# Kernel tuning notes

Hardware: AMD Instinct MI355X
Metric: run time of the kernel (lower is better)

The kernel has to match this reference:

```python
import jax, jax.numpy as jnp
import numpy as np

B, I, L, D, E, H, HR, A = 4096, 512, 128, 512, 8, 512, 256, 32


def setup_inputs() -> dict:
    key = jax.random.key(0)
    ks = jax.random.split(key, 12)
    s = 0.05
    n = lambda k, shape: (jax.random.normal(k, shape, jnp.float32) * s)
    return {
        "x": jax.random.normal(ks[0], (B, I), jnp.float32),
        "lang_embs": jax.random.normal(ks[1], (B, L), jnp.float32),
        "h_router": jnp.zeros((B, HR), jnp.float32),
        "h_experts": jnp.zeros((E, B, H), jnp.float32),
        # input projection Linear(I+L -> D)
        "W_in": n(ks[2], (D, I + L)), "b_in": jnp.zeros((D,), jnp.float32),
        # router GRU cell (PyTorch layout: rows ordered [r, z, n])
        "Wih_r": n(ks[3], (3 * HR, D)), "Whh_r": n(ks[4], (3 * HR, HR)),
        "bih_r": jnp.zeros((3 * HR,), jnp.float32), "bhh_r": jnp.zeros((3 * HR,), jnp.float32),
        # router fc Linear(HR -> E)
        "W_fc": n(ks[5], (E, HR)), "b_fc": jnp.zeros((E,), jnp.float32),
        # stacked expert GRU cells
        "Wih_e": n(ks[6], (E, 3 * H, D)), "Whh_e": n(ks[7], (E, 3 * H, H)),
        "bih_e": jnp.zeros((E, 3 * H), jnp.float32), "bhh_e": jnp.zeros((E, 3 * H), jnp.float32),
        # stacked expert projections Linear(H -> D)
        "W_proj": n(ks[8], (E, D, H)), "b_proj": jnp.zeros((E, D), jnp.float32),
        # head Linear(D -> A)
        "W_head": n(ks[9], (A, D)), "b_head": jnp.zeros((A,), jnp.float32),
    }


def _gru_cell(gx, gh, h):
    """Single GRU step given precomputed input/hidden gate pre-activations.
    gx, gh: (..., 3H) ordered [r, z, n]; h: (..., H)."""
    Hh = h.shape[-1]
    r = jax.nn.sigmoid(gx[..., :Hh] + gh[..., :Hh])
    z = jax.nn.sigmoid(gx[..., Hh:2 * Hh] + gh[..., Hh:2 * Hh])
    nct = jnp.tanh(gx[..., 2 * Hh:] + r * gh[..., 2 * Hh:])
    return (1.0 - z) * nct + z * h


def reference(x, lang_embs, h_router, h_experts,
              W_in, b_in, Wih_r, Whh_r, bih_r, bhh_r, W_fc, b_fc,
              Wih_e, Whh_e, bih_e, bhh_e, W_proj, b_proj, W_head, b_head):
    # input projection: (B, I+L) -> (B, D)
    xp = jnp.concatenate([x, lang_embs], axis=1) @ W_in.T + b_in

    # router GRU step + softmax weights
    gx_r = xp @ Wih_r.T + bih_r                      # (B, 3HR)
    gh_r = h_router @ Whh_r.T + bhh_r                # (B, 3HR)
    h_router_new = _gru_cell(gx_r, gh_r, h_router)   # (B, HR)
    weights = jax.nn.softmax(h_router_new @ W_fc.T + b_fc, axis=-1)  # (B, E)

    # all expert GRU steps fused into batched einsums over the expert dim
    gx_e = jnp.einsum('bd,egd->ebg', xp, Wih_e) + bih_e[:, None, :]        # (E, B, 3H)
    gh_e = jnp.einsum('ebh,egh->ebg', h_experts, Whh_e) + bhh_e[:, None, :]
    h_experts_new = _gru_cell(gx_e, gh_e, h_experts)                        # (E, B, H)

    # per-expert projection back to intermediate dim, then router-weighted sum
    expert_out = jnp.einsum('ebh,edh->ebd', h_experts_new, W_proj) + b_proj[:, None, :]
    combined = jnp.einsum('ebd,be->bd', expert_out, weights)               # (B, D)

    logits = combined @ W_head.T + b_head                                  # (B, A)
    return (logits, h_router_new, h_experts_new)
```

## Files before the change

### kernel.cpp

```cpp
#include <hip/hip_runtime.h>
#include <cstddef>
#include <cstdint>

#define B_  4096
#define I_  512
#define L_  128
#define D_  512
#define E_  8
#define H_  512
#define HR_ 256
#define A_  32

typedef __attribute__((ext_vector_type(8))) __bf16 bf16x8;
typedef __attribute__((ext_vector_type(4))) __bf16 bf16x4;
typedef __attribute__((ext_vector_type(4))) float floatx4;

__device__ __forceinline__ float sigmoidf_(float x) { return 1.0f / (1.0f + __expf(-x)); }

__device__ __forceinline__ void load_lds16(const void* g, void* l) {
    __builtin_amdgcn_global_load_lds((__attribute__((address_space(1))) void*)g,
                                     (__attribute__((address_space(3))) void*)l, 16, 0, 0);
}

struct HiLo { __bf16 h, l; };
__device__ __forceinline__ HiLo hi_lo(float v) {
    HiLo r;
    r.h = (__bf16)v;
    r.l = (__bf16)(v - (float)r.h);
    return r;
}
__device__ __forceinline__ void split4(float4 v, bf16x4& hi, bf16x4& lo) {
    HiLo a = hi_lo(v.x), b = hi_lo(v.y), c = hi_lo(v.z), d = hi_lo(v.w);
    hi = (bf16x4){a.h, b.h, c.h, d.h};
    lo = (bf16x4){a.l, b.l, c.l, d.l};
}

__device__ __forceinline__ int stage_seg(int lane) {
    return (lane & 3) ^ ((lane >> 3) & 3);
}
__device__ __forceinline__ int frag_off(int lane) {
    const int r = lane & 15, q = lane >> 4;
    return (r * 4 + (q ^ ((r >> 1) & 3))) * 8;
}

__global__ __launch_bounds__(256) void f2b_k(const float* __restrict__ src,
                                             __bf16* __restrict__ dst, int n4) {
    int i = blockIdx.x * 256 + threadIdx.x;
    if (i < n4) {
        float4 v = ((const float4*)src)[i];
        bf16x4 o = { (__bf16)v.x, (__bf16)v.y, (__bf16)v.z, (__bf16)v.w };
        *(bf16x4*)(dst + (size_t)i * 4) = o;
    }
}

__global__ __launch_bounds__(256) void wcat2_k(const float* __restrict__ W,
                                               __bf16* __restrict__ out,
                                               int K4, int n4tot) {
    int i4 = blockIdx.x * 256 + threadIdx.x;
    if (i4 >= n4tot) return;
    int row = i4 / K4;
    int c4  = i4 - row * K4;
    const int K = K4 * 4;
    float4 v = ((const float4*)W)[i4];
    bf16x4 hi, lo;
    split4(v, hi, lo);
    __bf16* dst = out + (size_t)row * 2 * K + c4 * 4;
    *(bf16x4*)(dst)     = hi;
    *(bf16x4*)(dst + K) = lo;
}

__global__ __launch_bounds__(256) void concat_cat_k(const float* __restrict__ x,
                                                    const float* __restrict__ lang,
                                                    __bf16* __restrict__ out) {
    int idx = blockIdx.x * 256 + threadIdx.x;
    int b = idx / 160;
    int c = idx - b * 160;
    float4 v;
    if (c < 128) v = ((const float4*)x)[(size_t)b * 128 + c];
    else         v = ((const float4*)lang)[(size_t)b * 32 + (c - 128)];
    bf16x4 hi, lo;
    split4(v, hi, lo);
    __bf16* dst = out + (size_t)b * 1920 + c * 4;
    *(bf16x4*)(dst)        = hi;
    *(bf16x4*)(dst + 640)  = hi;
    *(bf16x4*)(dst + 1280) = lo;
}

__global__ __launch_bounds__(256) void split2cat_k(const float* __restrict__ src,
                                                   __bf16* __restrict__ out) {
    int i4 = blockIdx.x * 256 + threadIdx.x;
    int b = i4 >> 7;
    int c4 = i4 & 127;
    float4 v = ((const float4*)src)[i4];
    bf16x4 hi, lo;
    split4(v, hi, lo);
    __bf16* dst = out + (size_t)b * 1536 + c4 * 4;
    *(bf16x4*)(dst)         = hi;
    *(bf16x4*)(dst + 512)   = hi;
    *(bf16x4*)(dst + 1024)  = lo;
}

__global__ __launch_bounds__(256) void f2bhe_k(const float* __restrict__ he,
                                               __bf16* __restrict__ dst, int r0) {
    int i4 = blockIdx.x * 256 + threadIdx.x;
    int e   = i4 >> 18;
    int rem = i4 & 262143;
    int row = rem >> 7;
    int c4  = rem & 127;
    float4 v = ((const float4*)he)[(size_t)e * (B_ * 128) + (size_t)(r0 + row) * 128 + c4];
    bf16x4 o = { (__bf16)v.x, (__bf16)v.y, (__bf16)v.z, (__bf16)v.w };
    *(bf16x4*)(dst + (size_t)i4 * 4) = o;
}

template<int MODE, bool XORD>
__global__ __launch_bounds__(256) void mgemm(
    const __bf16* __restrict__ A, long long aBatch,
    const __bf16* __restrict__ Bw, long long bBatch, int bRS, int kWrap,
    const float* __restrict__ bias, long long biasBatch,
    float* __restrict__ Cv, long long cBatch,
    int N, int K,
    const float* __restrict__ scale, int sstride, int szBatch)
{
    constexpr int ASZ = 128 * 32;
    __shared__ __align__(16) __bf16 As[2 * ASZ];
    __shared__ __align__(16) __bf16 Bs[2 * ASZ];

    const int tid  = threadIdx.x;
    const int w    = tid >> 6;
    const int lane = tid & 63;
    const int m0 = (XORD ? blockIdx.z : blockIdx.x) * 128;
    const int n0 = blockIdx.y * 128;
    const int z  = XORD ? blockIdx.x : blockIdx.z;

    const int lrow = lane >> 2;
    const int lsegx = stage_seg(lane);
    const __bf16* Ag0 = A + (size_t)z * aBatch + (size_t)(m0 + w * 32 + lrow) * K + lsegx * 8;
    const __bf16* Ag1 = Ag0 + (size_t)16 * K;
    const __bf16* Bg0 = Bw + (size_t)z * bBatch + (size_t)(n0 + w * 32 + lrow) * bRS + lsegx * 8;
    const __bf16* Bg1 = Bg0 + (size_t)16 * bRS;

    const int wm = w & 1, wn = w >> 1;
    const int lr16 = lane & 15;
    const int lq   = lane >> 4;
    const int fro  = frag_off(lane);

    floatx4 acc[4][4];
#pragma unroll
    for (int i = 0; i < 4; ++i)
#pragma unroll
        for (int j = 0; j < 4; ++j) acc[i][j] = (floatx4){0.f, 0.f, 0.f, 0.f};

    const int NSTEP = K >> 5;

    auto STAGE = [&](int s, int buf) {
        const int k0 = s << 5;
        const int kb = (k0 < kWrap) ? k0 : (k0 - kWrap);
        __bf16* al = As + buf * ASZ + (w * 32) * 32;
        __bf16* bl = Bs + buf * ASZ + (w * 32) * 32;
        load_lds16(Ag0 + k0, al);
        load_lds16(Ag1 + k0, al + 16 * 32);
        load_lds16(Bg0 + kb, bl);
        load_lds16(Bg1 + kb, bl + 16 * 32);
    };

    int cur = 0;
    STAGE(0, 0);
    __syncthreads();
    for (int s = 0; s < NSTEP; ++s) {
        if (s + 1 < NSTEP) STAGE(s + 1, cur ^ 1);

        const __bf16* Af = As + cur * ASZ + wm * 2048 + fro;
        const __bf16* Bf = Bs + cur * ASZ + wn * 2048 + fro;
        bf16x8 af[4], bfr[4];
#pragma unroll
        for (int t = 0; t < 4; ++t) {
            af[t]  = *(const bf16x8*)(Af + t * 512);
            bfr[t] = *(const bf16x8*)(Bf + t * 512);
        }
#pragma unroll
        for (int tm = 0; tm < 4; ++tm)
#pragma unroll
            for (int tn = 0; tn < 4; ++tn)
                acc[tm][tn] = __builtin_amdgcn_mfma_f32_16x16x32_bf16(af[tm], bfr[tn], acc[tm][tn], 0, 0, 0);

        __syncthreads();
        cur ^= 1;
    }

    const float* biasz = bias + (size_t)z * biasBatch;
    const int sz = z * szBatch;
#pragma unroll
    for (int tm = 0; tm < 4; ++tm) {
        const int mbase = m0 + wm * 64 + tm * 16 + lq * 4;
#pragma unroll
        for (int r = 0; r < 4; ++r) {
            const int m = mbase + r;
            float wsc = 0.f;
            if (MODE == 2) wsc = scale[(size_t)m * sstride + sz];
#pragma unroll
            for (int tn = 0; tn < 4; ++tn) {
                const int n = n0 + wn * 64 + tn * 16 + lr16;
                float v = acc[tm][tn][r] + biasz[n];
                const size_t ci = (size_t)z * cBatch + (size_t)m * N + n;
                if (MODE == 0) Cv[ci] = v;
                else           Cv[ci] = wsc * v;
            }
        }
    }
}

template<int HD, bool WRITE_HNEW, bool XORD>
__global__ __launch_bounds__(256) void fgru(
    const __bf16* __restrict__ Ab, long long aBatch,
    const __bf16* __restrict__ Whh, long long wBatch,
    const float* __restrict__ bhh, long long bhhBatch,
    const float* __restrict__ gx, long long gxBatch,
    const float* __restrict__ hprev, long long hBatch,
    float* __restrict__ hout, long long hoBatch,
    __bf16* __restrict__ hnew, long long hnBatch)
{
    __shared__ __align__(16) __bf16 As[128 * 32];
    __shared__ __align__(16) __bf16 Bs[192 * 32];

    const int tid  = threadIdx.x;
    const int w    = tid >> 6;
    const int lane = tid & 63;
    const int m0 = (XORD ? blockIdx.z : blockIdx.x) * 128;
    const int j0 = blockIdx.y * 64;
    const int z  = XORD ? blockIdx.x : blockIdx.z;

    const int lrow = lane >> 2;
    const int lsegx = stage_seg(lane);
    const __bf16* Ag0 = Ab + (size_t)z * aBatch + (size_t)(m0 + w * 32 + lrow) * HD + lsegx * 8;
    const __bf16* Ag1 = Ag0 + (size_t)16 * HD;
    __bf16* Al0 = As + (w * 32) * 32;
    __bf16* Al1 = Al0 + 16 * 32;

    const __bf16* Wz = Whh + (size_t)z * wBatch;
    const __bf16* Bg[3];
    __bf16* Bl[3];
#pragma unroll
    for (int i = 0; i < 3; ++i) {
        const int r = (w * 3 + i) * 16 + lrow;
        const int gate = r >> 6;
        const int grow = gate * HD + j0 + (r & 63);
        Bg[i] = Wz + (size_t)grow * HD + lsegx * 8;
        Bl[i] = Bs + ((w * 3 + i) * 16) * 32;
    }

    const int mh = w & 1, nh = w >> 1;
    const int lr16 = lane & 15;
    const int lq   = lane >> 4;
    const int fro  = frag_off(lane);
    const __bf16* Af = As + mh * 2048 + fro;
    const __bf16* Bf = Bs + nh * 1024 + fro;

    floatx4 acc[3][4][2];
#pragma unroll
    for (int g = 0; g < 3; ++g)
#pragma unroll
        for (int i = 0; i < 4; ++i)
#pragma unroll
            for (int j = 0; j < 2; ++j) acc[g][i][j] = (floatx4){0.f, 0.f, 0.f, 0.f};

    for (int k0 = 0; k0 < HD; k0 += 32) {
        __syncthreads();
        load_lds16(Ag0 + k0, Al0);
        load_lds16(Ag1 + k0, Al1);
#pragma unroll
        for (int i = 0; i < 3; ++i) load_lds16(Bg[i] + k0, Bl[i]);
        __syncthreads();

        bf16x8 af[4], bf[3][2];
#pragma unroll
        for (int t = 0; t < 4; ++t) af[t] = *(const bf16x8*)(Af + t * 512);
#pragma unroll
        for (int g = 0; g < 3; ++g)
#pragma unroll
            for (int tn = 0; tn < 2; ++tn)
                bf[g][tn] = *(const bf16x8*)(Bf + (g * 4 + tn) * 512);
#pragma unroll
        for (int g = 0; g < 3; ++g)
#pragma unroll
            for (int tm = 0; tm < 4; ++tm)
#pragma unroll
                for (int tn = 0; tn < 2; ++tn)
                    acc[g][tm][tn] = __builtin_amdgcn_mfma_f32_16x16x32_bf16(af[tm], bf[g][tn], acc[g][tm][tn], 0, 0, 0);
    }

    const float* bhhz = bhh + (size_t)z * bhhBatch;
#pragma unroll
    for (int tm = 0; tm < 4; ++tm) {
#pragma unroll
        for (int rr = 0; rr < 4; ++rr) {
            const int row = m0 + mh * 64 + tm * 16 + lq * 4 + rr;
            const float* gxrow = gx + (size_t)z * gxBatch + (size_t)row * (3 * HD);
            const float* hrow  = hprev + (size_t)z * hBatch + (size_t)row * HD;
#pragma unroll
            for (int tn = 0; tn < 2; ++tn) {
                const int j = j0 + nh * 32 + tn * 16 + lr16;
                float ghr = acc[0][tm][tn][rr] + bhhz[j];
                float ghz = acc[1][tm][tn][rr] + bhhz[HD + j];
                float ghn = acc[2][tm][tn][rr] + bhhz[2 * HD + j];
                float r  = sigmoidf_(gxrow[j] + ghr);
                float zz = sigmoidf_(gxrow[HD + j] + ghz);
                float n  = tanhf(gxrow[2 * HD + j] + r * ghn);
                float hv = hrow[j];
                float o  = (1.f - zz) * n + zz * hv;
                hout[(size_t)z * hoBatch + (size_t)row * HD + j] = o;
                if (WRITE_HNEW)
                    hnew[(size_t)z * hnBatch + (size_t)row * HD + j] = (__bf16)o;
            }
        }
    }
}

template<int MROWS>
__global__ __launch_bounds__(256, 2) void fxgru_k(
    const __bf16* __restrict__ xpc,
    const __bf16* __restrict__ Wih,
    const float* __restrict__ bih,
    const __bf16* __restrict__ heb,
    const __bf16* __restrict__ Whh,
    const float* __restrict__ bhh,
    const float* __restrict__ hprev,
    long long hBatch,
    float* __restrict__ hout,
    long long hoBatch,
    __bf16* __restrict__ hnew)
{
    constexpr int ASZ = 128 * 32;
    constexpr int BSZ = 192 * 32;
    __shared__ __align__(16) __bf16 As[3 * ASZ];
    __shared__ __align__(16) __bf16 Bs[3 * BSZ];

    const int tid  = threadIdx.x;
    const int w    = tid >> 6;
    const int lane = tid & 63;
    const int z  = blockIdx.x;
    const int j0 = blockIdx.y * 64;
    const int m0 = blockIdx.z * 128;

    const int lrow = lane >> 2;
    const int lsegx = stage_seg(lane);
    const int aoff = (w * 32) * 32;
    int BlOff[3];
#pragma unroll
    for (int i = 0; i < 3; ++i) BlOff[i] = ((w * 3 + i) * 16) * 32;

    const int mh = w & 1, nh = w >> 1;
    const int lr16 = lane & 15;
    const int lq   = lane >> 4;
    const int fro  = frag_off(lane);

    floatx4 acc[3][4][2];
    floatx4 accn[4][2];
#pragma unroll
    for (int g = 0; g < 3; ++g)
#pragma unroll
        for (int i = 0; i < 4; ++i)
#pragma unroll
            for (int j = 0; j < 2; ++j) acc[g][i][j] = (floatx4){0.f, 0.f, 0.f, 0.f};
#pragma unroll
    for (int i = 0; i < 4; ++i)
#pragma unroll
        for (int j = 0; j < 2; ++j) accn[i][j] = (floatx4){0.f, 0.f, 0.f, 0.f};

    auto COMPA = [&](int buf) {
        const __bf16* Af = As + buf * ASZ + mh * 2048 + fro;
        const __bf16* Bf = Bs + buf * BSZ + nh * 1024 + fro;
        bf16x8 af[4], bf[3][2];
#pragma unroll
        for (int t = 0; t < 4; ++t) af[t] = *(const bf16x8*)(Af + t * 512);
#pragma unroll
        for (int g = 0; g < 3; ++g)
#pragma unroll
            for (int tn = 0; tn < 2; ++tn)
                bf[g][tn] = *(const bf16x8*)(Bf + (g * 4 + tn) * 512);
#pragma unroll
        for (int g = 0; g < 3; ++g)
#pragma unroll
            for (int tm = 0; tm < 4; ++tm)
#pragma unroll
                for (int tn = 0; tn < 2; ++tn)
                    acc[g][tm][tn] = __builtin_amdgcn_mfma_f32_16x16x32_bf16(af[tm], bf[g][tn], acc[g][tm][tn], 0, 0, 0);
    };
    auto COMPB = [&](int buf) {
        const __bf16* Af = As + buf * ASZ + mh * 2048 + fro;
        const __bf16* Bf = Bs + buf * BSZ + nh * 1024 + fro;
        bf16x8 af[4], bf[3][2];
#pragma unroll
        for (int t = 0; t < 4; ++t) af[t] = *(const bf16x8*)(Af + t * 512);
#pragma unroll
        for (int g = 0; g < 3; ++g)
#pragma unroll
            for (int tn = 0; tn < 2; ++tn)
                bf[g][tn] = *(const bf16x8*)(Bf + (g * 4 + tn) * 512);
#pragma unroll
        for (int tm = 0; tm < 4; ++tm)
#pragma unroll
            for (int tn = 0; tn < 2; ++tn) {
                acc[0][tm][tn] = __builtin_amdgcn_mfma_f32_16x16x32_bf16(af[tm], bf[0][tn], acc[0][tm][tn], 0, 0, 0);
                acc[1][tm][tn] = __builtin_amdgcn_mfma_f32_16x16x32_bf16(af[tm], bf[1][tn], acc[1][tm][tn], 0, 0, 0);
                accn[tm][tn]   = __builtin_amdgcn_mfma_f32_16x16x32_bf16(af[tm], bf[2][tn], accn[tm][tn], 0, 0, 0);
            }
    };

#define TILE_WAIT(N) do { \
        asm volatile("s_waitcnt vmcnt(" #N ")" ::: "memory"); \
        __builtin_amdgcn_s_barrier(); \
        __builtin_amdgcn_sched_barrier(0); \
    } while (0)
#define READ_DONE() do { \
        __builtin_amdgcn_sched_barrier(0); \
        __builtin_amdgcn_s_barrier(); \
    } while (0)

    int cur = 0;
    {
        const __bf16* AgA0 = xpc + (size_t)(m0 + w * 32 + lrow) * 1536 + lsegx * 8;
        const __bf16* AgA1 = AgA0 + (size_t)16 * 1536;
        const __bf16* WihZ = Wih + (size_t)z * (1536 * 1024);
        const __bf16* BgA[3];
#pragma unroll
        for (int i = 0; i < 3; ++i) {
            const int r = (w * 3 + i) * 16 + lrow;
            const int grow = (r >> 6) * 512 + j0 + (r & 63);
            BgA[i] = WihZ + (size_t)grow * 1024 + lsegx * 8;
        }
        auto STAGE_A = [&](int s, int buf) {
            const int k0 = s << 5;
            const int kb = (k0 < 1024) ? k0 : (k0 - 1024);
            __bf16* al = As + buf * ASZ + aoff;
            __bf16* bl = Bs + buf * BSZ;
            load_lds16(AgA0 + k0, al);
            load_lds16(AgA1 + k0, al + 16 * 32);
#pragma unroll
            for (int i = 0; i < 3; ++i) load_lds16(BgA[i] + kb, bl + BlOff[i]);
        };

        STAGE_A(0, 0);
        STAGE_A(1, 1);
        STAGE_A(2, 2);
        for (int s = 0; s < 45; ++s) {
            TILE_WAIT(10);
            COMPA(cur);
            READ_DONE();
            STAGE_A(s + 3, cur);
            cur = (cur == 2) ? 0 : cur + 1;
        }
    }
    {
        const __bf16* AgB0 = heb + (size_t)z * (MROWS * 512)
                                 + (size_t)(m0 + w * 32 + lrow) * 512 + lsegx * 8;
        const __bf16* AgB1 = AgB0 + (size_t)16 * 512;
        const __bf16* WhhZ = Whh + (size_t)z * (1536 * 512);
        const __bf16* BgB[3];
#pragma unroll
        for (int i = 0; i < 3; ++i) {
            const int r = (w * 3 + i) * 16 + lrow;
            const int grow = (r >> 6) * 512 + j0 + (r & 63);
            BgB[i] = WhhZ + (size_t)grow * 512 + lsegx * 8;
        }
        auto STAGE_B = [&](int t, int buf) {
            const int k0 = t << 5;
            __bf16* al = As + buf * ASZ + aoff;
            __bf16* bl = Bs + buf * BSZ;
            load_lds16(AgB0 + k0, al);
            load_lds16(AgB1 + k0, al + 16 * 32);
#pragma unroll
            for (int i = 0; i < 3; ++i) load_lds16(BgB[i] + k0, bl + BlOff[i]);
        };

#pragma unroll
        for (int q = 0; q < 3; ++q) {
            TILE_WAIT(10);
            COMPA(cur);
            READ_DONE();
            STAGE_B(q, cur);
            cur = (cur == 2) ? 0 : cur + 1;
        }
        for (int t = 0; t < 13; ++t) {
            TILE_WAIT(10);
            COMPB(cur);
            READ_DONE();
            STAGE_B(t + 3, cur);
            cur = (cur == 2) ? 0 : cur + 1;
        }
        TILE_WAIT(10);
        COMPB(cur);
        cur = (cur == 2) ? 0 : cur + 1;
        TILE_WAIT(5);
        COMPB(cur);
        cur = (cur == 2) ? 0 : cur + 1;
        TILE_WAIT(0);
        COMPB(cur);
    }
#undef TILE_WAIT
#undef READ_DONE

    const float* bihz = bih + (size_t)z * 1536;
    const float* bhhz = bhh + (size_t)z * 1536;
#pragma unroll
    for (int tm = 0; tm < 4; ++tm) {
#pragma unroll
        for (int rr = 0; rr < 4; ++rr) {
            const int row = m0 + mh * 64 + tm * 16 + lq * 4 + rr;
            const float* hrow = hprev + (size_t)z * hBatch + (size_t)row * 512;
#pragma unroll
            for (int tn = 0; tn < 2; ++tn) {
                const int j = j0 + nh * 32 + tn * 16 + lr16;
                float gr  = acc[0][tm][tn][rr] + bihz[j] + bhhz[j];
                float gz  = acc[1][tm][tn][rr] + bihz[512 + j] + bhhz[512 + j];
                float gxn = acc[2][tm][tn][rr] + bihz[1024 + j];
                float ghn = accn[tm][tn][rr] + bhhz[1024 + j];
                float r  = sigmoidf_(gr);
                float zz = sigmoidf_(gz);
                float n  = tanhf(gxn + r * ghn);
                float hv = hrow[j];
                float o  = (1.f - zz) * n + zz * hv;
                hout[(size_t)z * hoBatch + (size_t)row * 512 + j] = o;
                hnew[(size_t)z * (MROWS * 512) + (size_t)row * 512 + j] = (__bf16)o;
            }
        }
    }
}

__global__ __launch_bounds__(256) void fc_softmax_k(const float* __restrict__ hr,
                                                    const float* __restrict__ Wfc,
                                                    const float* __restrict__ bfc,
                                                    float* __restrict__ wts) {
    int lane = threadIdx.x & 63;
    int wave = threadIdx.x >> 6;
    int rg = lane >> 3;
    int e  = lane & 7;
    int b  = blockIdx.x * 32 + wave * 8 + rg;
    const float* h = hr + (size_t)b * HR_;
    const float* w = Wfc + (size_t)e * HR_;
    float acc = 0.0f;
#pragma unroll 4
    for (int k = 0; k < HR_; k += 4) {
        float4 hv = *(const float4*)(h + k);
        float4 wv = *(const float4*)(w + k);
        acc += hv.x * wv.x + hv.y * wv.y + hv.z * wv.z + hv.w * wv.w;
    }
    acc += bfc[e];
    float m = acc;
    for (int off = 4; off; off >>= 1) m = fmaxf(m, __shfl_xor(m, off, 8));
    float ex = __expf(acc - m);
    float s = ex;
    for (int off = 4; off; off >>= 1) s += __shfl_xor(s, off, 8);
    wts[(size_t)b * E_ + e] = ex / s;
}

__global__ __launch_bounds__(256) void reduce8_k(const float* __restrict__ P,
                                                 float* __restrict__ comb,
                                                 int n4, int ps4) {
    int i = blockIdx.x * 256 + threadIdx.x;
    if (i >= n4) return;
    float4 s = ((const float4*)P)[i];
#pragma unroll
    for (int e = 1; e < E_; ++e) {
        float4 v = ((const float4*)P)[i + (size_t)e * ps4];
        s.x += v.x; s.y += v.y; s.z += v.z; s.w += v.w;
    }
    ((float4*)comb)[i] = s;
}

__global__ __launch_bounds__(256) void head_k(const float* __restrict__ comb,
                                              const float* __restrict__ Wh,
                                              const float* __restrict__ bh,
                                              float* __restrict__ out) {
    __shared__ float hs[8][512];
    int b0 = blockIdx.x * 8;
    for (int i = threadIdx.x; i < 8 * 128; i += 256) {
        int rr = i >> 7, cc = i & 127;
        ((float4*)hs[rr])[cc] = ((const float4*)(comb + (size_t)(b0 + rr) * 512))[cc];
    }
    __syncthreads();
    int r = threadIdx.x >> 5, c = threadIdx.x & 31;
    const float* wrow = Wh + (size_t)c * 512;
    float acc = 0.f;
    for (int k = 0; k < 512; k += 4) {
        float4 wv = *(const float4*)(wrow + k);
        float4 hv = *(const float4*)(&hs[r][k]);
        acc += hv.x * wv.x + hv.y * wv.y + hv.z * wv.z + hv.w * wv.w;
    }
    out[(size_t)(b0 + r) * 32 + c] = acc + bh[c];
}

extern "C" void kernel_launch(void* const* d_in, const int* in_sizes, int n_in,
                              void* d_out, int out_size, void* d_ws, size_t ws_size,
                              hipStream_t stream)
{
    const float* x      = (const float*)d_in[0];
    const float* lang   = (const float*)d_in[1];
    const float* h_r    = (const float*)d_in[2];
    const float* h_e    = (const float*)d_in[3];
    const float* W_in   = (const float*)d_in[4];
    const float* b_in   = (const float*)d_in[5];
    const float* Wih_r  = (const float*)d_in[6];
    const float* Whh_r  = (const float*)d_in[7];
    const float* bih_r  = (const float*)d_in[8];
    const float* bhh_r  = (const float*)d_in[9];
    const float* W_fc   = (const float*)d_in[10];
    const float* b_fc   = (const float*)d_in[11];
    const float* Wih_e  = (const float*)d_in[12];
    const float* Whh_e  = (const float*)d_in[13];
    const float* bih_e  = (const float*)d_in[14];
    const float* bhh_e  = (const float*)d_in[15];
    const float* W_proj = (const float*)d_in[16];
    const float* b_proj = (const float*)d_in[17];
    const float* W_head = (const float*)d_in[18];
    const float* b_head = (const float*)d_in[19];

    float* out_logits = (float*)d_out;
    float* out_hr     = out_logits + (size_t)B_ * A_;
    float* out_he     = out_hr + (size_t)B_ * HR_;

    char* wsb = (char*)d_ws;
    size_t off = 0;
    auto alloc = [&](size_t bytes) -> char* {
        char* p = wsb + off;
        off = (off + bytes + 255) & ~(size_t)255;
        return p;
    };

    __bf16* Wih_e_hl = (__bf16*)alloc((size_t)12288 * 1024 * 2);
    __bf16* Whh_e_b  = (__bf16*)alloc((size_t)8 * 1536 * 512 * 2);
    __bf16* W_proj_b = (__bf16*)alloc((size_t)8 * 512 * 512 * 2);
    __bf16* xp_cat   = (__bf16*)alloc((size_t)B_ * 1536 * 2);
    float*  wts      = (float*)alloc((size_t)B_ * E_ * 4);
    float*  comb     = (float*)alloc((size_t)B_ * D_ * 4);

    char* R = wsb + off;
    __bf16* W_in_hl  = (__bf16*)(R);
    __bf16* Wih_r_hl = (__bf16*)(R + 1310720);
    __bf16* Whh_r_b  = (__bf16*)(R + 1310720 + 1572864);
    __bf16* hr_b     = (__bf16*)(R + 1310720 + 1572864 + 393216);
    char*   Rp       = R + 1310720 + 1572864 + 393216 + 2097152;
    __bf16* xcat_cat = (__bf16*)(Rp);
    float*  xp       = (float*)(Rp + 15728640);
    float*  gxr      = (float*)(Rp + 15728640 + 8388608);
    float*  Pch      = (float*)(R);
    __bf16* hebch    = (__bf16*)(R + 33554432);
    __bf16* henewch  = (__bf16*)(R + 33554432 + 16777216);

    wcat2_k<<<(512 * 160 + 255) / 256, 256, 0, stream>>>(W_in, W_in_hl, 160, 512 * 160);
    wcat2_k<<<(768 * 128 + 255) / 256, 256, 0, stream>>>(Wih_r, Wih_r_hl, 128, 768 * 128);
    wcat2_k<<<(12288 * 128 + 255) / 256, 256, 0, stream>>>(Wih_e, Wih_e_hl, 128, 12288 * 128);
    f2b_k<<<(49152 + 255) / 256, 256, 0, stream>>>(Whh_r, Whh_r_b, 49152);
    f2b_k<<<(1572864 + 255) / 256, 256, 0, stream>>>(Whh_e, Whh_e_b, 1572864);
    f2b_k<<<(524288 + 255) / 256, 256, 0, stream>>>(W_proj, W_proj_b, 524288);
    f2b_k<<<(262144 + 255) / 256, 256, 0, stream>>>(h_r, hr_b, 262144);

    concat_cat_k<<<(B_ * 160) / 256, 256, 0, stream>>>(x, lang, xcat_cat);
    mgemm<0, false><<<dim3(32, 4, 1), 256, 0, stream>>>(xcat_cat, 0, W_in_hl, 0, 1280, 1280,
                                                        b_in, 0, xp, 0, D_, 1920, nullptr, 0, 0);
    split2cat_k<<<(B_ * 128) / 256, 256, 0, stream>>>(xp, xp_cat);

    mgemm<0, false><<<dim3(32, 6, 1), 256, 0, stream>>>(xp_cat, 0, Wih_r_hl, 0, 1024, 1024,
                                                        bih_r, 0, gxr, 0, 3 * HR_, 1536, nullptr, 0, 0);
    fgru<HR_, false, false><<<dim3(32, 4, 1), 256, 0, stream>>>(
        hr_b, 0, Whh_r_b, 0, bhh_r, 0, gxr, 0, h_r, 0, out_hr, 0, nullptr, 0);
    fc_softmax_k<<<B_ / 32, 256, 0, stream>>>(out_hr, W_fc, b_fc, wts);

    for (int c = 0; c < 2; ++c) {
        const int r0 = c * 2048;
        f2bhe_k<<<(8 * 2048 * 128) / 256, 256, 0, stream>>>(h_e, hebch, r0);
        fxgru_k<2048><<<dim3(8, 8, 16), 256, 0, stream>>>(
            xp_cat + (size_t)r0 * 1536,
            Wih_e_hl, bih_e,
            hebch, Whh_e_b, bhh_e,
            h_e + (size_t)r0 * H_, (long long)B_ * H_,
            out_he + (size_t)r0 * H_, (long long)B_ * H_,
            henewch);
        mgemm<2, true><<<dim3(8, 4, 16), 256, 0, stream>>>(
            henewch, (long long)2048 * H_,
            W_proj_b, (long long)D_ * H_, 512, 512,
            b_proj, D_,
            Pch, (long long)2048 * D_, D_, H_,
            wts + (size_t)r0 * E_, E_, 1);
        reduce8_k<<<(2048 * 128 + 255) / 256, 256, 0, stream>>>(
            Pch, comb + (size_t)r0 * D_, 2048 * 128, 2048 * 128);
    }

    head_k<<<B_ / 8, 256, 0, stream>>>(comb, W_head, b_head, out_logits);
}
```

Baseline: 672.4 us.

## Fuse prep conversions into one kernel and use smaller-tile GEMM for front layers

Merges all weight and input fp32-to-bf16 conversion kernels into a single launch. Adds a 64x128-tile double-buffered GEMM for the input projection and the router input GEMM, so the grid has more blocks. The input projection GEMM now writes the hi/lo bf16 split layout directly in its epilogue, removing the fp32 intermediate and the separate split kernel. This cuts launch count and one round trip through memory, at the cost of scattered 2-byte stores in the epilogue.

```diff
diff --git a/kernel.cpp b/kernel.cpp
--- a/kernel.cpp
+++ b/kernel.cpp
@@ -43,61 +43,88 @@
     return (r * 4 + (q ^ ((r >> 1) & 3))) * 8;
 }
 
-__global__ __launch_bounds__(256) void f2b_k(const float* __restrict__ src,
-                                             __bf16* __restrict__ dst, int n4) {
+__global__ __launch_bounds__(256) void prep_all_k(
+    const float* __restrict__ W_in,  const float* __restrict__ Wih_r,
+    const float* __restrict__ Wih_e, const float* __restrict__ Whh_r,
+    const float* __restrict__ Whh_e, const float* __restrict__ W_proj,
+    const float* __restrict__ h_r,
+    const float* __restrict__ x,     const float* __restrict__ lang,
+    __bf16* __restrict__ W_in_hl,  __bf16* __restrict__ Wih_r_hl,
+    __bf16* __restrict__ Wih_e_hl, __bf16* __restrict__ Whh_r_b,
+    __bf16* __restrict__ Whh_e_b,  __bf16* __restrict__ W_proj_b,
+    __bf16* __restrict__ hr_b,     __bf16* __restrict__ xcat)
+{
     int i = blockIdx.x * 256 + threadIdx.x;
-    if (i < n4) {
-        float4 v = ((const float4*)src)[i];
+
+    if (i < 1572864) {
+        int row = i >> 7, c4 = i & 127;
+        float4 v = ((const float4*)Wih_e)[i];
+        bf16x4 hi, lo; split4(v, hi, lo);
+        __bf16* dst = Wih_e_hl + (size_t)row * 1024 + c4 * 4;
+        *(bf16x4*)(dst)       = hi;
+        *(bf16x4*)(dst + 512) = lo;
+        return;
+    }
+    i -= 1572864;
+    if (i < 1572864) {
+        float4 v = ((const float4*)Whh_e)[i];
         bf16x4 o = { (__bf16)v.x, (__bf16)v.y, (__bf16)v.z, (__bf16)v.w };
-        *(bf16x4*)(dst + (size_t)i * 4) = o;
-    }
-}
-
-__global__ __launch_bounds__(256) void wcat2_k(const float* __restrict__ W,
-                                               __bf16* __restrict__ out,
-                                               int K4, int n4tot) {
-    int i4 = blockIdx.x * 256 + threadIdx.x;
-    if (i4 >= n4tot) return;
-    int row = i4 / K4;
-    int c4  = i4 - row * K4;
-    const int K = K4 * 4;
-    float4 v = ((const float4*)W)[i4];
-    bf16x4 hi, lo;
-    split4(v, hi, lo);
-    __bf16* dst = out + (size_t)row * 2 * K + c4 * 4;
-    *(bf16x4*)(dst)     = hi;
-    *(bf16x4*)(dst + K) = lo;
-}
-
-__global__ __launch_bounds__(256) void concat_cat_k(const float* __restrict__ x,
-                                                    const float* __restrict__ lang,
-                                                    __bf16* __restrict__ out) {
-    int idx = blockIdx.x * 256 + threadIdx.x;
-    int b = idx / 160;
-    int c = idx - b * 160;
-    float4 v;
-    if (c < 128) v = ((const float4*)x)[(size_t)b * 128 + c];
-    else         v = ((const float4*)lang)[(size_t)b * 32 + (c - 128)];
-    bf16x4 hi, lo;
-    split4(v, hi, lo);
-    __bf16* dst = out + (size_t)b * 1920 + c * 4;
-    *(bf16x4*)(dst)        = hi;
-    *(bf16x4*)(dst + 640)  = hi;
-    *(bf16x4*)(dst + 1280) = lo;
-}
-
-__global__ __launch_bounds__(256) void split2cat_k(const float* __restrict__ src,
-                                                   __bf16* __restrict__ out) {
-    int i4 = blockIdx.x * 256 + threadIdx.x;
-    int b = i4 >> 7;
-    int c4 = i4 & 127;
-    float4 v = ((const float4*)src)[i4];
-    bf16x4 hi, lo;
-    split4(v, hi, lo);
-    __bf16* dst = out + (size_t)b * 1536 + c4 * 4;
-    *(bf16x4*)(dst)         = hi;
-    *(bf16x4*)(dst + 512)   = hi;
-    *(bf16x4*)(dst + 1024)  = lo;
+        *(bf16x4*)(Whh_e_b + (size_t)i * 4) = o;
+        return;
+    }
+    i -= 1572864;
+    if (i < 655360) {
+        int b = i / 160, c = i - b * 160;
+        float4 v;
+        if (c < 128) v = ((const float4*)x)[(size_t)b * 128 + c];
+        else         v = ((const float4*)lang)[(size_t)b * 32 + (c - 128)];
+        bf16x4 hi, lo; split4(v, hi, lo);
+        __bf16* dst = xcat + (size_t)b * 1920 + c * 4;
+        *(bf16x4*)(dst)        = hi;
+        *(bf16x4*)(dst + 640)  = hi;
+        *(bf16x4*)(dst + 1280) = lo;
+        return;
+    }
+    i -= 655360;
+    if (i < 524288) {
+        float4 v = ((const float4*)W_proj)[i];
+        bf16x4 o = { (__bf16)v.x, (__bf16)v.y, (__bf16)v.z, (__bf16)v.w };
+        *(bf16x4*)(W_proj_b + (size_t)i * 4) = o;
+        return;
+    }
+    i -= 524288;
+    if (i < 262144) {
+        float4 v = ((const float4*)h_r)[i];
+        bf16x4 o = { (__bf16)v.x, (__bf16)v.y, (__bf16)v.z, (__bf16)v.w };
+        *(bf16x4*)(hr_b + (size_t)i * 4) = o;
+        return;
+    }
+    i -= 262144;
+    if (i < 98304) {
+        int row = i >> 7, c4 = i & 127;
+        float4 v = ((const float4*)Wih_r)[i];
+        bf16x4 hi, lo; split4(v, hi, lo);
+        __bf16* dst = Wih_r_hl + (size_t)row * 1024 + c4 * 4;
+        *(bf16x4*)(dst)       = hi;
+        *(bf16x4*)(dst + 512) = lo;
+        return;
+    }
+    i -= 98304;
+    if (i < 81920) {
+        int row = i / 160, c4 = i - row * 160;
+        float4 v = ((const float4*)W_in)[i];
+        bf16x4 hi, lo; split4(v, hi, lo);
+        __bf16* dst = W_in_hl + (size_t)row * 1280 + c4 * 4;
+        *(bf16x4*)(dst)       = hi;
+        *(bf16x4*)(dst + 640) = lo;
+        return;
+    }
+    i -= 81920;
+    if (i < 49152) {
+        float4 v = ((const float4*)Whh_r)[i];
+        bf16x4 o = { (__bf16)v.x, (__bf16)v.y, (__bf16)v.z, (__bf16)v.w };
+        *(bf16x4*)(Whh_r_b + (size_t)i * 4) = o;
+    }
 }
 
 __global__ __launch_bounds__(256) void f2bhe_k(const float* __restrict__ he,
@@ -204,6 +231,99 @@
                 const size_t ci = (size_t)z * cBatch + (size_t)m * N + n;
                 if (MODE == 0) Cv[ci] = v;
                 else           Cv[ci] = wsc * v;
+            }
+        }
+    }
+}
+
+template<int MODE>
+__global__ __launch_bounds__(256) void mgemm64(
+    const __bf16* __restrict__ A,
+    const __bf16* __restrict__ Bw, int bRS, int kWrap,
+    const float* __restrict__ bias,
+    void* __restrict__ Cv,
+    int N, int K)
+{
+    constexpr int ASZ = 64 * 32;
+    constexpr int BSZ = 128 * 32;
+    __shared__ __align__(16) __bf16 As[2 * ASZ];
+    __shared__ __align__(16) __bf16 Bs[2 * BSZ];
+
+    const int tid  = threadIdx.x;
+    const int w    = tid >> 6;
+    const int lane = tid & 63;
+    const int m0 = blockIdx.x * 64;
+    const int n0 = blockIdx.y * 128;
+
+    const int lrow = lane >> 2;
+    const int lsegx = stage_seg(lane);
+    const __bf16* Ag  = A + (size_t)(m0 + w * 16 + lrow) * K + lsegx * 8;
+    const __bf16* Bg0 = Bw + (size_t)(n0 + w * 32 + lrow) * bRS + lsegx * 8;
+    const __bf16* Bg1 = Bg0 + (size_t)16 * bRS;
+
+    const int lr16 = lane & 15;
+    const int lq   = lane >> 4;
+    const int fro  = frag_off(lane);
+
+    floatx4 acc[4][2];
+#pragma unroll
+    for (int i = 0; i < 4; ++i)
+#pragma unroll
+        for (int j = 0; j < 2; ++j) acc[i][j] = (floatx4){0.f, 0.f, 0.f, 0.f};
+
+    const int NSTEP = K >> 5;
+
+    auto STAGE = [&](int s, int buf) {
+        const int k0 = s << 5;
+        const int kb = (k0 < kWrap) ? k0 : (k0 - kWrap);
+        __bf16* al = As + buf * ASZ + w * 512;
+        __bf16* bl = Bs + buf * BSZ + (w * 2) * 512;
+        load_lds16(Ag + k0, al);
+        load_lds16(Bg0 + kb, bl);
+        load_lds16(Bg1 + kb, bl + 512);
+    };
+
+    int cur = 0;
+    STAGE(0, 0);
+    __syncthreads();
+    for (int s = 0; s < NSTEP; ++s) {
+        if (s + 1 < NSTEP) STAGE(s + 1, cur ^ 1);
+
+        const __bf16* Af = As + cur * ASZ + fro;
+        const __bf16* Bf = Bs + cur * BSZ + (w * 2) * 512 + fro;
+        bf16x8 af[4], bfr[2];
+#pragma unroll
+        for (int t = 0; t < 4; ++t) af[t] = *(const bf16x8*)(Af + t * 512);
+#pragma unroll
+        for (int t = 0; t < 2; ++t) bfr[t] = *(const bf16x8*)(Bf + t * 512);
+#pragma unroll
+        for (int tm = 0; tm < 4; ++tm)
+#pragma unroll
+            for (int tn = 0; tn < 2; ++tn)
+                acc[tm][tn] = __builtin_amdgcn_mfma_f32_16x16x32_bf16(af[tm], bfr[tn], acc[tm][tn], 0, 0, 0);
+
+        __syncthreads();
+        cur ^= 1;
+    }
+
+#pragma unroll
+    for (int tm = 0; tm < 4; ++tm) {
+#pragma unroll
+        for (int r = 0; r < 4; ++r) {
+            const int m = m0 + tm * 16 + lq * 4 + r;
+#pragma unroll
+            for (int tn = 0; tn < 2; ++tn) {
+                const int n = n0 + w * 32 + tn * 16 + lr16;
+                float v = acc[tm][tn][r] + bias[n];
+                if (MODE == 0) {
+                    ((float*)Cv)[(size_t)m * N + n] = v;
+                } else {
+                    HiLo hl = hi_lo(v);
+                    __bf16* xc = (__bf16*)Cv + (size_t)m * 1536 + n;
+                    xc[0]    = hl.h;
+                    xc[512]  = hl.h;
+                    xc[1024] = hl.l;
+                }
             }
         }
     }
@@ -640,27 +760,20 @@
     __bf16* hr_b     = (__bf16*)(R + 1310720 + 1572864 + 393216);
     char*   Rp       = R + 1310720 + 1572864 + 393216 + 2097152;
     __bf16* xcat_cat = (__bf16*)(Rp);
-    float*  xp       = (float*)(Rp + 15728640);
     float*  gxr      = (float*)(Rp + 15728640 + 8388608);
     float*  Pch      = (float*)(R);
     __bf16* hebch    = (__bf16*)(R + 33554432);
     __bf16* henewch  = (__bf16*)(R + 33554432 + 16777216);
 
-    wcat2_k<<<(512 * 160 + 255) / 256, 256, 0, stream>>>(W_in, W_in_hl, 160, 512 * 160);
-    wcat2_k<<<(768 * 128 + 255) / 256, 256, 0, stream>>>(Wih_r, Wih_r_hl, 128, 768 * 128);
-    wcat2_k<<<(12288 * 128 + 255) / 256, 256, 0, stream>>>(Wih_e, Wih_e_hl, 128, 12288 * 128);
-    f2b_k<<<(49152 + 255) / 256, 256, 0, stream>>>(Whh_r, Whh_r_b, 49152);
-    f2b_k<<<(1572864 + 255) / 256, 256, 0, stream>>>(Whh_e, Whh_e_b, 1572864);
-    f2b_k<<<(524288 + 255) / 256, 256, 0, stream>>>(W_proj, W_proj_b, 524288);
-    f2b_k<<<(262144 + 255) / 256, 256, 0, stream>>>(h_r, hr_b, 262144);
-
-    concat_cat_k<<<(B_ * 160) / 256, 256, 0, stream>>>(x, lang, xcat_cat);
-    mgemm<0, false><<<dim3(32, 4, 1), 256, 0, stream>>>(xcat_cat, 0, W_in_hl, 0, 1280, 1280,
-                                                        b_in, 0, xp, 0, D_, 1920, nullptr, 0, 0);
-    split2cat_k<<<(B_ * 128) / 256, 256, 0, stream>>>(xp, xp_cat);
-
-    mgemm<0, false><<<dim3(32, 6, 1), 256, 0, stream>>>(xp_cat, 0, Wih_r_hl, 0, 1024, 1024,
-                                                        bih_r, 0, gxr, 0, 3 * HR_, 1536, nullptr, 0, 0);
+    prep_all_k<<<18816, 256, 0, stream>>>(
+        W_in, Wih_r, Wih_e, Whh_r, Whh_e, W_proj, h_r, x, lang,
+        W_in_hl, Wih_r_hl, Wih_e_hl, Whh_r_b, Whh_e_b, W_proj_b, hr_b, xcat_cat);
+
+    mgemm64<3><<<dim3(64, 4), 256, 0, stream>>>(
+        xcat_cat, W_in_hl, 1280, 1280, b_in, xp_cat, 512, 1920);
+
+    mgemm64<0><<<dim3(64, 6), 256, 0, stream>>>(
+        xp_cat, Wih_r_hl, 1024, 1024, bih_r, gxr, 768, 1536);
     fgru<HR_, false, false><<<dim3(32, 4, 1), 256, 0, stream>>>(
         hr_b, 0, Whh_r_b, 0, bhh_r, 0, gxr, 0, h_r, 0, out_hr, 0, nullptr, 0);
     fc_softmax_k<<<B_ / 32, 256, 0, stream>>>(out_hr, W_fc, b_fc, wts);
```

After: 635.3 us. -5.5%, faster.
